# Performance work log

Measured on AMD Instinct MI355X. Metric: run time of the kernel, lower is better.

## Reference

```python
import jax, jax.numpy as jnp
import numpy as np

B, S, Lb, C, CP, H = 64, 4, 64, 32, 16, 4
LN_EPS = 1e-5


def layer_norm(x, g, b):
    mu = jnp.mean(x, axis=-1, keepdims=True)
    var = jnp.mean(jnp.square(x - mu), axis=-1, keepdims=True)
    return (x - mu) * jax.lax.rsqrt(var + LN_EPS) * g + b


def mha(x, w_in, b_in, w_out, b_out, h):
    # torch nn.MultiheadAttention, batch_first, self-attention
    Bx, L, Cx = x.shape
    d = Cx // h
    qkv = x @ w_in.T + b_in                      # (Bx, L, 3C)
    q, k, v = jnp.split(qkv, 3, axis=-1)
    sp = lambda t: t.reshape(Bx, L, h, d).transpose(0, 2, 1, 3)  # (Bx,h,L,d)
    q, k, v = sp(q), sp(k), sp(v)
    scale = 1.0 / jnp.sqrt(jnp.asarray(d, x.dtype))
    attn = jax.nn.softmax(jnp.einsum('bhid,bhjd->bhij', q, k) * scale, axis=-1)
    o = jnp.einsum('bhij,bhjd->bhid', attn, v).transpose(0, 2, 1, 3).reshape(Bx, L, Cx)
    return o @ w_out.T + b_out


def setup_inputs() -> dict:
    key = jax.random.key(0)
    ks = jax.random.split(key, 20)
    g = lambda i, shape, s=0.05: (jax.random.normal(ks[i], shape, dtype=jnp.float32) * s)
    inp = {
        'chip_ctcf': jax.random.normal(ks[0], (B, Lb), dtype=jnp.float32),
        'chip_hac':  jax.random.normal(ks[1], (B, Lb), dtype=jnp.float32),
        'chip_me1':  jax.random.normal(ks[2], (B, Lb), dtype=jnp.float32),
        'chip_me3':  jax.random.normal(ks[3], (B, Lb), dtype=jnp.float32),
        'embed_w': g(4, (C, 1)), 'embed_b': g(5, (C,)),
        'pos_embed': g(6, (1, 1, Lb, C), 0.02),
        'row_in_w': g(7, (3 * C, C)), 'row_in_b': g(8, (3 * C,)),
        'row_out_w': g(9, (C, C)), 'row_out_b': g(10, (C,)),
        'row_ln_g': jnp.ones((C,), jnp.float32), 'row_ln_b': jnp.zeros((C,), jnp.float32),
        'col_in_w': g(11, (3 * C, C)), 'col_in_b': g(12, (3 * C,)),
        'col_out_w': g(13, (C, C)), 'col_out_b': g(14, (C,)),
        'col_ln_g': jnp.ones((C,), jnp.float32), 'col_ln_b': jnp.zeros((C,), jnp.float32),
        'proj_w': g(15, (CP, C * C)), 'proj_b': g(16, (CP,)),
        'pln_g': jnp.ones((CP,), jnp.float32), 'pln_b': jnp.zeros((CP,), jnp.float32),
    }
    return inp


def reference(chip_ctcf, chip_hac, chip_me1, chip_me3,
              embed_w, embed_b, pos_embed,
              row_in_w, row_in_b, row_out_w, row_out_b, row_ln_g, row_ln_b,
              col_in_w, col_in_b, col_out_w, col_out_b, col_ln_g, col_ln_b,
              proj_w, proj_b, pln_g, pln_b):
    Bv = chip_ctcf.shape[0]
    signals = jnp.stack([chip_ctcf, chip_hac, chip_me1, chip_me3], axis=1)  # (B,4,64)
    # Linear(1, C): scalar embed
    msa = signals[..., None] * embed_w[:, 0] + embed_b                      # (B,4,64,C)
    msa = msa + pos_embed
    # row attention over the 64 bins, per track
    x = msa.reshape(Bv * S, Lb, C)
    x = layer_norm(x + mha(x, row_in_w, row_in_b, row_out_w, row_out_b, H), row_ln_g, row_ln_b)
    msa = x.reshape(Bv, S, Lb, C)
    # column attention over the 4 tracks, per bin
    x = msa.transpose(0, 2, 1, 3).reshape(Bv * Lb, S, C)
    x = layer_norm(x + mha(x, col_in_w, col_in_b, col_out_w, col_out_b, H), col_ln_g, col_ln_b)
    msa = x.reshape(Bv, Lb, S, C).transpose(0, 2, 1, 3)                     # (B,4,64,C)
    # outer product of the track-mean (as written in the torch source)
    m = jnp.mean(msa, axis=1)                                               # (B,64,C)
    pair = jnp.einsum('bic,bjd->bijcd', m, m).reshape(Bv, Lb, Lb, C * C)    # (B,64,64,1024)
    nrm = jnp.sqrt(jnp.sum(jnp.square(pair), axis=-1, keepdims=True))
    pair = pair / jnp.maximum(nrm, 1e-6)                                    # F.normalize eps=1e-6
    feat = pair @ proj_w.T + proj_b                                         # (B,64,64,CP)
    feat = layer_norm(feat, pln_g, pln_b)
    feat = feat * jax.nn.sigmoid(feat)                                      # SiLU
    return feat.transpose(0, 3, 1, 2)                                       # (B,CP,64,64)
```

## Files before the change

kernel.cpp:

```cpp
#include <hip/hip_runtime.h>

#define LN_EPS 1e-5f

__device__ __forceinline__ float dot8(float4 a0, float4 a1, float4 b0, float4 b1) {
    return a0.x * b0.x + a0.y * b0.y + a0.z * b0.z + a0.w * b0.w +
           a1.x * b1.x + a1.y * b1.y + a1.z * b1.z + a1.w * b1.w;
}

__global__ __launch_bounds__(1024) void k_row(
    const float* __restrict__ ctcf, const float* __restrict__ hac,
    const float* __restrict__ me1,  const float* __restrict__ me3,
    const float* __restrict__ ew,   const float* __restrict__ eb,
    const float* __restrict__ pe,
    const float* __restrict__ w_in, const float* __restrict__ b_in,
    const float* __restrict__ w_out,const float* __restrict__ b_out,
    const float* __restrict__ ln_g, const float* __restrict__ ln_b,
    float* __restrict__ msaR)
{
    __shared__ float sx[64][33];
    __shared__ float sqkv[64 * 100];
    __shared__ float so[64][33];
    __shared__ float smean[64], srstd[64];

    const int blk = blockIdx.x;
    const int s   = blk & 3;
    const int b   = blk >> 2;
    const int tid = threadIdx.x;

    const float* chip = (s == 0) ? ctcf : (s == 1) ? hac : (s == 2) ? me1 : me3;

    for (int n = tid; n < 2048; n += 1024) {
        int l = n >> 5, c = n & 31;
        sx[l][c] = chip[b * 64 + l] * ew[c] + eb[c] + pe[l * 32 + c];
    }
    __syncthreads();

    const int l  = tid & 63;
    const int cg = tid >> 6;

    {
        float xr[32];
#pragma unroll
        for (int c = 0; c < 32; ++c) xr[c] = sx[l][c];
#pragma unroll
        for (int i = 0; i < 6; ++i) {
            int cc = i * 16 + cg;
            const float4* wr4 = (const float4*)&w_in[cc * 32];
            float acc = b_in[cc];
#pragma unroll
            for (int c4 = 0; c4 < 8; ++c4) {
                float4 wv = wr4[c4];
                acc += xr[c4 * 4 + 0] * wv.x + xr[c4 * 4 + 1] * wv.y +
                       xr[c4 * 4 + 2] * wv.z + xr[c4 * 4 + 3] * wv.w;
            }
            sqkv[l * 100 + cc] = acc;
        }
    }
    __syncthreads();

    {
        const int h  = tid >> 8;
        const int la = (tid >> 2) & 63;
        const int kc = tid & 3;
        const float4* qp = (const float4*)&sqkv[la * 100 + h * 8];
        float4 q0 = qp[0], q1 = qp[1];
        const float scale = 0.35355339059327373f;
        float mrun = -1e30f, denom = 0.f, a[8];
#pragma unroll
        for (int dd = 0; dd < 8; ++dd) a[dd] = 0.f;
#pragma unroll
        for (int jj = 0; jj < 16; ++jj) {
            const int j = kc * 16 + jj;
            const float4* kp = (const float4*)&sqkv[j * 100 + 32 + h * 8];
            float sc = dot8(q0, q1, kp[0], kp[1]) * scale;
            const float4* vp = (const float4*)&sqkv[j * 100 + 64 + h * 8];
            float4 v0 = vp[0], v1 = vp[1];
            float mnew = fmaxf(mrun, sc);
            float corr = __expf(mrun - mnew);
            float w = __expf(sc - mnew);
            denom = denom * corr + w;
            a[0] = a[0] * corr + w * v0.x;  a[1] = a[1] * corr + w * v0.y;
            a[2] = a[2] * corr + w * v0.z;  a[3] = a[3] * corr + w * v0.w;
            a[4] = a[4] * corr + w * v1.x;  a[5] = a[5] * corr + w * v1.y;
            a[6] = a[6] * corr + w * v1.z;  a[7] = a[7] * corr + w * v1.w;
            mrun = mnew;
        }
#pragma unroll
        for (int off = 1; off <= 2; off <<= 1) {
            float mo = __shfl_xor(mrun, off, 64);
            float dn = __shfl_xor(denom, off, 64);
            float mn = fmaxf(mrun, mo);
            float c1 = __expf(mrun - mn);
            float c2 = __expf(mo - mn);
            denom = denom * c1 + dn * c2;
#pragma unroll
            for (int dd = 0; dd < 8; ++dd) {
                float ao = __shfl_xor(a[dd], off, 64);
                a[dd] = a[dd] * c1 + ao * c2;
            }
            mrun = mn;
        }
        float inv = 1.f / denom;
        float r0, r1;
        if      (kc == 0) { r0 = a[0]; r1 = a[1]; }
        else if (kc == 1) { r0 = a[2]; r1 = a[3]; }
        else if (kc == 2) { r0 = a[4]; r1 = a[5]; }
        else              { r0 = a[6]; r1 = a[7]; }
        so[la][h * 8 + kc * 2 + 0] = r0 * inv;
        so[la][h * 8 + kc * 2 + 1] = r1 * inv;
    }
    __syncthreads();

    {
        float orow[32];
#pragma unroll
        for (int k = 0; k < 32; ++k) orow[k] = so[l][k];
#pragma unroll
        for (int i = 0; i < 2; ++i) {
            int c = i * 16 + cg;
            const float4* wr4 = (const float4*)&w_out[c * 32];
            float acc = b_out[c] + sx[l][c];
#pragma unroll
            for (int k4 = 0; k4 < 8; ++k4) {
                float4 wv = wr4[k4];
                acc += orow[k4 * 4 + 0] * wv.x + orow[k4 * 4 + 1] * wv.y +
                       orow[k4 * 4 + 2] * wv.z + orow[k4 * 4 + 3] * wv.w;
            }
            sqkv[l * 100 + c] = acc;
        }
    }
    __syncthreads();

    if (tid < 64) {
        float mu = 0.f;
#pragma unroll
        for (int c = 0; c < 32; ++c) mu += sqkv[tid * 100 + c];
        mu *= (1.f / 32.f);
        float var = 0.f;
#pragma unroll
        for (int c = 0; c < 32; ++c) { float d = sqkv[tid * 100 + c] - mu; var += d * d; }
        var *= (1.f / 32.f);
        smean[tid] = mu;
        srstd[tid] = rsqrtf(var + LN_EPS);
    }
    __syncthreads();

    float* outp = msaR + blk * 2048;
    for (int n = tid; n < 2048; n += 1024) {
        int ll = n >> 5, c = n & 31;
        outp[n] = (sqkv[ll * 100 + c] - smean[ll]) * srstd[ll] * ln_g[c] + ln_b[c];
    }
}

__global__ __launch_bounds__(1024) void k_col(
    const float* __restrict__ msaR,
    const float* __restrict__ w_in, const float* __restrict__ b_in,
    const float* __restrict__ w_out,const float* __restrict__ b_out,
    const float* __restrict__ ln_g, const float* __restrict__ ln_b,
    float* __restrict__ m_out, float* __restrict__ nrm_out)
{
    __shared__ float sx[64][33];
    __shared__ float sqkv[64 * 100];
    __shared__ float so[64][33];
    __shared__ float smean2[64], srstd2[64];
    __shared__ float smv[16][33];

    const int bx = blockIdx.x;
    const int b  = bx >> 2;
    const int l0 = (bx & 3) * 16;
    const int tid = threadIdx.x;

    for (int n = tid; n < 2048; n += 1024) {
        int s = n >> 9, lo = (n >> 5) & 15, c = n & 31;
        sx[s * 16 + lo][c] = msaR[((b * 4 + s) * 64 + l0 + lo) * 32 + c];
    }
    __syncthreads();

    const int r  = tid & 63;
    const int sS = r & 3, lo = r >> 2;
    const int cg = tid >> 6;

    {
        float xr[32];
#pragma unroll
        for (int c = 0; c < 32; ++c) xr[c] = sx[sS * 16 + lo][c];
#pragma unroll
        for (int i = 0; i < 6; ++i) {
            int cc = i * 16 + cg;
            const float4* wr4 = (const float4*)&w_in[cc * 32];
            float acc = b_in[cc];
#pragma unroll
            for (int c4 = 0; c4 < 8; ++c4) {
                float4 wv = wr4[c4];
                acc += xr[c4 * 4 + 0] * wv.x + xr[c4 * 4 + 1] * wv.y +
                       xr[c4 * 4 + 2] * wv.z + xr[c4 * 4 + 3] * wv.w;
            }
            sqkv[r * 100 + cc] = acc;
        }
    }
    __syncthreads();

    if (tid < 256) {
        const int la = tid >> 4, h = (tid >> 2) & 3, ia = tid & 3;
        const float scale = 0.35355339059327373f;
        const float4* qp = (const float4*)&sqkv[(la * 4 + ia) * 100 + h * 8];
        float4 q0 = qp[0], q1 = qp[1];
        float sc[4];
        float mx = -1e30f;
#pragma unroll
        for (int jj = 0; jj < 4; ++jj) {
            const float4* kp = (const float4*)&sqkv[(la * 4 + jj) * 100 + 32 + h * 8];
            sc[jj] = dot8(q0, q1, kp[0], kp[1]) * scale;
            mx = fmaxf(mx, sc[jj]);
        }
        float den = 0.f;
#pragma unroll
        for (int jj = 0; jj < 4; ++jj) { sc[jj] = __expf(sc[jj] - mx); den += sc[jj]; }
        float inv = 1.f / den;
        float a[8];
#pragma unroll
        for (int dd = 0; dd < 8; ++dd) a[dd] = 0.f;
#pragma unroll
        for (int jj = 0; jj < 4; ++jj) {
            const float4* vp = (const float4*)&sqkv[(la * 4 + jj) * 100 + 64 + h * 8];
            float4 v0 = vp[0], v1 = vp[1];
            float wgt = sc[jj];
            a[0] += wgt * v0.x;  a[1] += wgt * v0.y;
            a[2] += wgt * v0.z;  a[3] += wgt * v0.w;
            a[4] += wgt * v1.x;  a[5] += wgt * v1.y;
            a[6] += wgt * v1.z;  a[7] += wgt * v1.w;
        }
#pragma unroll
        for (int dd = 0; dd < 8; ++dd) so[la * 4 + ia][h * 8 + dd] = a[dd] * inv;
    }
    __syncthreads();

    {
        float orow[32];
#pragma unroll
        for (int k = 0; k < 32; ++k) orow[k] = so[r][k];
#pragma unroll
        for (int i = 0; i < 2; ++i) {
            int c = i * 16 + cg;
            const float4* wr4 = (const float4*)&w_out[c * 32];
            float acc = b_out[c] + sx[sS * 16 + lo][c];
#pragma unroll
            for (int k4 = 0; k4 < 8; ++k4) {
                float4 wv = wr4[k4];
                acc += orow[k4 * 4 + 0] * wv.x + orow[k4 * 4 + 1] * wv.y +
                       orow[k4 * 4 + 2] * wv.z + orow[k4 * 4 + 3] * wv.w;
            }
            sqkv[r * 100 + c] = acc;
        }
    }
    __syncthreads();

    if (tid < 64) {
        float mu = 0.f;
#pragma unroll
        for (int c = 0; c < 32; ++c) mu += sqkv[tid * 100 + c];
        mu *= (1.f / 32.f);
        float var = 0.f;
#pragma unroll
        for (int c = 0; c < 32; ++c) { float d = sqkv[tid * 100 + c] - mu; var += d * d; }
        var *= (1.f / 32.f);
        smean2[tid] = mu;
        srstd2[tid] = rsqrtf(var + LN_EPS);
    }
    __syncthreads();

    if (tid < 512) {
        int loo = tid >> 5, c = tid & 31;
        float acc = 0.f;
#pragma unroll
        for (int ss = 0; ss < 4; ++ss) {
            int rr = loo * 4 + ss;
            acc += (sqkv[rr * 100 + c] - smean2[rr]) * srstd2[rr];
        }
        float mval = 0.25f * acc * ln_g[c] + ln_b[c];
        m_out[(b * 64 + l0 + loo) * 32 + c] = mval;
        smv[loo][c] = mval * mval;
    }
    __syncthreads();

    if (tid < 16) {
        float sum = 0.f;
#pragma unroll
        for (int c = 0; c < 32; ++c) sum += smv[tid][c];
        nrm_out[b * 64 + l0 + tid] = sqrtf(sum);
    }
}

__global__ __launch_bounds__(512, 4) void k_pair(
    const float* __restrict__ m, const float* __restrict__ nrm,
    const float* __restrict__ pw, const float* __restrict__ pb,
    const float* __restrict__ pg, const float* __restrict__ pbeta,
    float* __restrict__ out)
{
    __shared__ float smj[64][36];
    __shared__ float sT[8 * 520];
    __shared__ float snj[64];
    __shared__ float sbias[16], sgam[16], sbet[16];

    const int bx = blockIdx.x;
    const int b  = bx >> 3;
    const int i0 = (bx & 7) * 8;
    const int tid = threadIdx.x;
    const int lane = tid & 63, w = tid >> 6;

    const int rem = tid;
    const float* pwp = pw + (rem >> 5) * 1024 + (rem & 31);
    float w0[32];
#pragma unroll
    for (int c = 0; c < 32; ++c) w0[c] = pwp[c * 32];

    const float* mb = m + b * 2048;
    for (int n = tid; n < 2048; n += 512) smj[n >> 5][n & 31] = mb[n];
    if (tid < 64) snj[tid] = nrm[b * 64 + tid];
    if (tid < 16) {
        sbias[tid] = pb[tid];
        sgam[tid]  = pg[tid];
        sbet[tid]  = pbeta[tid];
    }
    __syncthreads();

#pragma unroll
    for (int il = 0; il < 8; ++il) {
        const float4* mr4 = (const float4*)&smj[i0 + il][0];
        float a0 = 0.f;
#pragma unroll
        for (int c4 = 0; c4 < 8; ++c4) {
            float4 mv = mr4[c4];
            a0 += mv.x * w0[c4 * 4 + 0] + mv.y * w0[c4 * 4 + 1] +
                  mv.z * w0[c4 * 4 + 2] + mv.w * w0[c4 * 4 + 3];
        }
        sT[il * 520 + rem] = a0;
    }
    __syncthreads();

    const int j = lane;
    float mj[32];
    {
        const float4* mjp = (const float4*)&smj[j][0];
#pragma unroll
        for (int d4 = 0; d4 < 8; ++d4) {
            float4 t = mjp[d4];
            mj[d4 * 4 + 0] = t.x;  mj[d4 * 4 + 1] = t.y;
            mj[d4 * 4 + 2] = t.z;  mj[d4 * 4 + 3] = t.w;
        }
    }
    const float nj = snj[j];

    {
        const int il = w;
        const int ig = i0 + il;
        const float invn = 1.f / fmaxf(snj[ig] * nj, 1e-6f);
        float f[16];
#pragma unroll
        for (int cp = 0; cp < 16; ++cp) {
            const float4* tr = (const float4*)&sT[il * 520 + cp * 32];
            float acc = 0.f;
#pragma unroll
            for (int d4 = 0; d4 < 8; ++d4) {
                float4 tv = tr[d4];
                acc += tv.x * mj[d4 * 4 + 0] + tv.y * mj[d4 * 4 + 1] +
                       tv.z * mj[d4 * 4 + 2] + tv.w * mj[d4 * 4 + 3];
            }
            f[cp] = acc * invn + sbias[cp];
        }
        float mu = 0.f;
#pragma unroll
        for (int cp = 0; cp < 16; ++cp) mu += f[cp];
        mu *= (1.f / 16.f);
        float var = 0.f;
#pragma unroll
        for (int cp = 0; cp < 16; ++cp) { float d = f[cp] - mu; var += d * d; }
        var *= (1.f / 16.f);
        const float rstd = rsqrtf(var + LN_EPS);
#pragma unroll
        for (int cp = 0; cp < 16; ++cp) {
            float v = (f[cp] - mu) * rstd * sgam[cp] + sbet[cp];
            float sl = v / (1.f + __expf(-v));
            out[((b * 16 + cp) * 64 + ig) * 64 + j] = sl;
        }
    }
}

extern "C" void kernel_launch(void* const* d_in, const int* in_sizes, int n_in,
                              void* d_out, int out_size, void* d_ws, size_t ws_size,
                              hipStream_t stream) {
    const float* ctcf  = (const float*)d_in[0];
    const float* hac   = (const float*)d_in[1];
    const float* me1   = (const float*)d_in[2];
    const float* me3   = (const float*)d_in[3];
    const float* ew    = (const float*)d_in[4];
    const float* ebias = (const float*)d_in[5];
    const float* pe    = (const float*)d_in[6];
    const float* riw   = (const float*)d_in[7];
    const float* rib   = (const float*)d_in[8];
    const float* row_  = (const float*)d_in[9];
    const float* rob   = (const float*)d_in[10];
    const float* rlg   = (const float*)d_in[11];
    const float* rlb   = (const float*)d_in[12];
    const float* ciw   = (const float*)d_in[13];
    const float* cib   = (const float*)d_in[14];
    const float* cow   = (const float*)d_in[15];
    const float* cob   = (const float*)d_in[16];
    const float* clg   = (const float*)d_in[17];
    const float* clb   = (const float*)d_in[18];
    const float* pw    = (const float*)d_in[19];
    const float* pb    = (const float*)d_in[20];
    const float* pg    = (const float*)d_in[21];
    const float* pbt   = (const float*)d_in[22];

    float* out = (float*)d_out;

    float* msaR = (float*)d_out;
    float* mbuf = (float*)d_ws;
    float* nbuf = mbuf + 64 * 64 * 32;

    k_row<<<256, 1024, 0, stream>>>(ctcf, hac, me1, me3, ew, ebias, pe,
                                    riw, rib, row_, rob, rlg, rlb, msaR);
    k_col<<<256, 1024, 0, stream>>>(msaR, ciw, cib, cow, cob, clg, clb,
                                    mbuf, nbuf);
    k_pair<<<512, 512, 0, stream>>>(mbuf, nbuf, pw, pb, pg, pbt, out);
}
```

Measured before the change: 149.2 us.

## Split all three kernels into smaller blocks and use shuffle-based layer norm

```diff
diff --git a/kernel.cpp b/kernel.cpp
--- a/kernel.cpp
+++ b/kernel.cpp
@@ -7,7 +7,7 @@
            a1.x * b1.x + a1.y * b1.y + a1.z * b1.z + a1.w * b1.w;
 }
 
-__global__ __launch_bounds__(1024) void k_row(
+__global__ __launch_bounds__(512, 4) void k_row(
     const float* __restrict__ ctcf, const float* __restrict__ hac,
     const float* __restrict__ me1,  const float* __restrict__ me3,
     const float* __restrict__ ew,   const float* __restrict__ eb,
@@ -19,32 +19,32 @@
 {
     __shared__ float sx[64][33];
     __shared__ float sqkv[64 * 100];
-    __shared__ float so[64][33];
-    __shared__ float smean[64], srstd[64];
+    __shared__ float so[32][33];
 
     const int blk = blockIdx.x;
-    const int s   = blk & 3;
-    const int b   = blk >> 2;
+    const int qh  = blk & 1;
+    const int s   = (blk >> 1) & 3;
+    const int b   = blk >> 3;
+    const int qbase = qh * 32;
     const int tid = threadIdx.x;
 
     const float* chip = (s == 0) ? ctcf : (s == 1) ? hac : (s == 2) ? me1 : me3;
 
-    for (int n = tid; n < 2048; n += 1024) {
+    for (int n = tid; n < 2048; n += 512) {
         int l = n >> 5, c = n & 31;
         sx[l][c] = chip[b * 64 + l] * ew[c] + eb[c] + pe[l * 32 + c];
     }
     __syncthreads();
 
-    const int l  = tid & 63;
-    const int cg = tid >> 6;
-
-    {
+    {
+        const int l  = tid & 63;
+        const int cg = tid >> 6;
         float xr[32];
 #pragma unroll
         for (int c = 0; c < 32; ++c) xr[c] = sx[l][c];
 #pragma unroll
-        for (int i = 0; i < 6; ++i) {
-            int cc = i * 16 + cg;
+        for (int i = 0; i < 12; ++i) {
+            int cc = i * 8 + cg;
             const float4* wr4 = (const float4*)&w_in[cc * 32];
             float acc = b_in[cc];
 #pragma unroll
@@ -59,10 +59,11 @@
     __syncthreads();
 
     {
-        const int h  = tid >> 8;
-        const int la = (tid >> 2) & 63;
+        const int h  = tid >> 7;
+        const int q  = (tid >> 2) & 31;
         const int kc = tid & 3;
-        const float4* qp = (const float4*)&sqkv[la * 100 + h * 8];
+        const int lq = qbase + q;
+        const float4* qp = (const float4*)&sqkv[lq * 100 + h * 8];
         float4 q0 = qp[0], q1 = qp[1];
         const float scale = 0.35355339059327373f;
         float mrun = -1e30f, denom = 0.f, a[8];
@@ -70,7 +71,7 @@
         for (int dd = 0; dd < 8; ++dd) a[dd] = 0.f;
 #pragma unroll
         for (int jj = 0; jj < 16; ++jj) {
-            const int j = kc * 16 + jj;
+            const int j = kc * 16 + ((jj + kc) & 15);
             const float4* kp = (const float4*)&sqkv[j * 100 + 32 + h * 8];
             float sc = dot8(q0, q1, kp[0], kp[1]) * scale;
             const float4* vp = (const float4*)&sqkv[j * 100 + 64 + h * 8];
@@ -106,84 +107,82 @@
         else if (kc == 1) { r0 = a[2]; r1 = a[3]; }
         else if (kc == 2) { r0 = a[4]; r1 = a[5]; }
         else              { r0 = a[6]; r1 = a[7]; }
-        so[la][h * 8 + kc * 2 + 0] = r0 * inv;
-        so[la][h * 8 + kc * 2 + 1] = r1 * inv;
-    }
-    __syncthreads();
-
-    {
+        so[q][h * 8 + kc * 2 + 0] = r0 * inv;
+        so[q][h * 8 + kc * 2 + 1] = r1 * inv;
+    }
+    __syncthreads();
+
+    {
+        const int lq2 = tid & 31;
+        const int cB  = tid >> 5;
         float orow[32];
 #pragma unroll
-        for (int k = 0; k < 32; ++k) orow[k] = so[l][k];
+        for (int k = 0; k < 32; ++k) orow[k] = so[lq2][k];
 #pragma unroll
         for (int i = 0; i < 2; ++i) {
-            int c = i * 16 + cg;
+            int c = cB + i * 16;
             const float4* wr4 = (const float4*)&w_out[c * 32];
-            float acc = b_out[c] + sx[l][c];
+            float acc = b_out[c] + sx[qbase + lq2][c];
 #pragma unroll
             for (int k4 = 0; k4 < 8; ++k4) {
                 float4 wv = wr4[k4];
                 acc += orow[k4 * 4 + 0] * wv.x + orow[k4 * 4 + 1] * wv.y +
                        orow[k4 * 4 + 2] * wv.z + orow[k4 * 4 + 3] * wv.w;
             }
-            sqkv[l * 100 + c] = acc;
-        }
-    }
-    __syncthreads();
-
-    if (tid < 64) {
-        float mu = 0.f;
-#pragma unroll
-        for (int c = 0; c < 32; ++c) mu += sqkv[tid * 100 + c];
-        mu *= (1.f / 32.f);
-        float var = 0.f;
-#pragma unroll
-        for (int c = 0; c < 32; ++c) { float d = sqkv[tid * 100 + c] - mu; var += d * d; }
-        var *= (1.f / 32.f);
-        smean[tid] = mu;
-        srstd[tid] = rsqrtf(var + LN_EPS);
-    }
-    __syncthreads();
-
-    float* outp = msaR + blk * 2048;
-    for (int n = tid; n < 2048; n += 1024) {
-        int ll = n >> 5, c = n & 31;
-        outp[n] = (sqkv[ll * 100 + c] - smean[ll]) * srstd[ll] * ln_g[c] + ln_b[c];
+            sqkv[lq2 * 100 + c] = acc;
+        }
+    }
+    __syncthreads();
+
+    {
+        const int c = tid & 31;
+#pragma unroll
+        for (int p = 0; p < 2; ++p) {
+            int r = p * 16 + (tid >> 5);
+            float v = sqkv[r * 100 + c];
+            float s1 = v;
+#pragma unroll
+            for (int off = 16; off >= 1; off >>= 1) s1 += __shfl_xor(s1, off, 64);
+            float mu = s1 * (1.f / 32.f);
+            float d = v - mu;
+            float s2 = d * d;
+#pragma unroll
+            for (int off = 16; off >= 1; off >>= 1) s2 += __shfl_xor(s2, off, 64);
+            float rstd = rsqrtf(s2 * (1.f / 32.f) + LN_EPS);
+            msaR[((b * 4 + s) * 64 + qbase + r) * 32 + c] = d * rstd * ln_g[c] + ln_b[c];
+        }
     }
 }
 
-__global__ __launch_bounds__(1024) void k_col(
+__global__ __launch_bounds__(512, 4) void k_col(
     const float* __restrict__ msaR,
     const float* __restrict__ w_in, const float* __restrict__ b_in,
     const float* __restrict__ w_out,const float* __restrict__ b_out,
     const float* __restrict__ ln_g, const float* __restrict__ ln_b,
     float* __restrict__ m_out, float* __restrict__ nrm_out)
 {
-    __shared__ float sx[64][33];
-    __shared__ float sqkv[64 * 100];
-    __shared__ float so[64][33];
-    __shared__ float smean2[64], srstd2[64];
-    __shared__ float smv[16][33];
+    __shared__ float sx[32][33];
+    __shared__ float sqkv[32 * 100];
+    __shared__ float so[32][33];
 
     const int bx = blockIdx.x;
-    const int b  = bx >> 2;
-    const int l0 = (bx & 3) * 16;
+    const int b  = bx >> 3;
+    const int l0 = (bx & 7) * 8;
     const int tid = threadIdx.x;
 
-    for (int n = tid; n < 2048; n += 1024) {
-        int s = n >> 9, lo = (n >> 5) & 15, c = n & 31;
-        sx[s * 16 + lo][c] = msaR[((b * 4 + s) * 64 + l0 + lo) * 32 + c];
-    }
-    __syncthreads();
-
-    const int r  = tid & 63;
-    const int sS = r & 3, lo = r >> 2;
-    const int cg = tid >> 6;
-
-    {
+    for (int n = tid; n < 1024; n += 512) {
+        int r = n >> 5, c = n & 31;
+        int lo = r >> 2, s = r & 3;
+        sx[r][c] = msaR[((b * 4 + s) * 64 + l0 + lo) * 32 + c];
+    }
+    __syncthreads();
+
+    {
+        const int rr = tid & 31;
+        const int cg = tid >> 5;
         float xr[32];
 #pragma unroll
-        for (int c = 0; c < 32; ++c) xr[c] = sx[sS * 16 + lo][c];
+        for (int c = 0; c < 32; ++c) xr[c] = sx[rr][c];
 #pragma unroll
         for (int i = 0; i < 6; ++i) {
             int cc = i * 16 + cg;
@@ -195,21 +194,21 @@
                 acc += xr[c4 * 4 + 0] * wv.x + xr[c4 * 4 + 1] * wv.y +
                        xr[c4 * 4 + 2] * wv.z + xr[c4 * 4 + 3] * wv.w;
             }
-            sqkv[r * 100 + cc] = acc;
-        }
-    }
-    __syncthreads();
-
-    if (tid < 256) {
-        const int la = tid >> 4, h = (tid >> 2) & 3, ia = tid & 3;
+            sqkv[rr * 100 + cc] = acc;
+        }
+    }
+    __syncthreads();
+
+    if (tid < 128) {
+        const int lo = tid >> 4, h = (tid >> 2) & 3, ia = tid & 3;
         const float scale = 0.35355339059327373f;
-        const float4* qp = (const float4*)&sqkv[(la * 4 + ia) * 100 + h * 8];
+        const float4* qp = (const float4*)&sqkv[(lo * 4 + ia) * 100 + h * 8];
         float4 q0 = qp[0], q1 = qp[1];
         float sc[4];
         float mx = -1e30f;
 #pragma unroll
         for (int jj = 0; jj < 4; ++jj) {
-            const float4* kp = (const float4*)&sqkv[(la * 4 + jj) * 100 + 32 + h * 8];
+            const float4* kp = (const float4*)&sqkv[(lo * 4 + jj) * 100 + 32 + h * 8];
             sc[jj] = dot8(q0, q1, kp[0], kp[1]) * scale;
             mx = fmaxf(mx, sc[jj]);
         }
@@ -222,7 +221,7 @@
         for (int dd = 0; dd < 8; ++dd) a[dd] = 0.f;
 #pragma unroll
         for (int jj = 0; jj < 4; ++jj) {
-            const float4* vp = (const float4*)&sqkv[(la * 4 + jj) * 100 + 64 + h * 8];
+            const float4* vp = (const float4*)&sqkv[(lo * 4 + jj) * 100 + 64 + h * 8];
             float4 v0 = vp[0], v1 = vp[1];
             float wgt = sc[jj];
             a[0] += wgt * v0.x;  a[1] += wgt * v0.y;
@@ -231,91 +230,90 @@
             a[6] += wgt * v1.z;  a[7] += wgt * v1.w;
         }
 #pragma unroll
-        for (int dd = 0; dd < 8; ++dd) so[la * 4 + ia][h * 8 + dd] = a[dd] * inv;
-    }
-    __syncthreads();
-
-    {
+        for (int dd = 0; dd < 8; ++dd) so[lo * 4 + ia][h * 8 + dd] = a[dd] * inv;
+    }
+    __syncthreads();
+
+    {
+        const int r2 = tid & 31;
+        const int cB = tid >> 5;
         float orow[32];
 #pragma unroll
-        for (int k = 0; k < 32; ++k) orow[k] = so[r][k];
+        for (int k = 0; k < 32; ++k) orow[k] = so[r2][k];
 #pragma unroll
         for (int i = 0; i < 2; ++i) {
-            int c = i * 16 + cg;
+            int c = cB + i * 16;
             const float4* wr4 = (const float4*)&w_out[c * 32];
-            float acc = b_out[c] + sx[sS * 16 + lo][c];
+            float acc = b_out[c] + sx[r2][c];
 #pragma unroll
             for (int k4 = 0; k4 < 8; ++k4) {
                 float4 wv = wr4[k4];
                 acc += orow[k4 * 4 + 0] * wv.x + orow[k4 * 4 + 1] * wv.y +
                        orow[k4 * 4 + 2] * wv.z + orow[k4 * 4 + 3] * wv.w;
             }
-            sqkv[r * 100 + c] = acc;
-        }
-    }
-    __syncthreads();
-
-    if (tid < 64) {
-        float mu = 0.f;
-#pragma unroll
-        for (int c = 0; c < 32; ++c) mu += sqkv[tid * 100 + c];
-        mu *= (1.f / 32.f);
-        float var = 0.f;
-#pragma unroll
-        for (int c = 0; c < 32; ++c) { float d = sqkv[tid * 100 + c] - mu; var += d * d; }
-        var *= (1.f / 32.f);
-        smean2[tid] = mu;
-        srstd2[tid] = rsqrtf(var + LN_EPS);
-    }
-    __syncthreads();
-
-    if (tid < 512) {
-        int loo = tid >> 5, c = tid & 31;
-        float acc = 0.f;
-#pragma unroll
-        for (int ss = 0; ss < 4; ++ss) {
-            int rr = loo * 4 + ss;
-            acc += (sqkv[rr * 100 + c] - smean2[rr]) * srstd2[rr];
-        }
-        float mval = 0.25f * acc * ln_g[c] + ln_b[c];
-        m_out[(b * 64 + l0 + loo) * 32 + c] = mval;
-        smv[loo][c] = mval * mval;
-    }
-    __syncthreads();
-
-    if (tid < 16) {
-        float sum = 0.f;
-#pragma unroll
-        for (int c = 0; c < 32; ++c) sum += smv[tid][c];
-        nrm_out[b * 64 + l0 + tid] = sqrtf(sum);
+            sqkv[r2 * 100 + c] = acc;
+        }
+    }
+    __syncthreads();
+
+    {
+        const int c = tid & 31;
+#pragma unroll
+        for (int p = 0; p < 2; ++p) {
+            int r = p * 16 + (tid >> 5);
+            float v = sqkv[r * 100 + c];
+            float s1 = v;
+#pragma unroll
+            for (int off = 16; off >= 1; off >>= 1) s1 += __shfl_xor(s1, off, 64);
+            float mu = s1 * (1.f / 32.f);
+            float d = v - mu;
+            float s2 = d * d;
+#pragma unroll
+            for (int off = 16; off >= 1; off >>= 1) s2 += __shfl_xor(s2, off, 64);
+            float rstd = rsqrtf(s2 * (1.f / 32.f) + LN_EPS);
+            so[r][c] = d * rstd;
+        }
+    }
+    __syncthreads();
+
+    if (tid < 256) {
+        const int lo = tid >> 5, c = tid & 31;
+        float mval = 0.25f * (so[lo * 4 + 0][c] + so[lo * 4 + 1][c] +
+                              so[lo * 4 + 2][c] + so[lo * 4 + 3][c]) * ln_g[c] + ln_b[c];
+        m_out[(b * 64 + l0 + lo) * 32 + c] = mval;
+        float q2 = mval * mval;
+#pragma unroll
+        for (int off = 16; off >= 1; off >>= 1) q2 += __shfl_xor(q2, off, 64);
+        if (c == 0) nrm_out[b * 64 + l0 + lo] = sqrtf(q2);
     }
 }
 
-__global__ __launch_bounds__(512, 4) void k_pair(
+__global__ __launch_bounds__(256, 4) void k_pair(
     const float* __restrict__ m, const float* __restrict__ nrm,
     const float* __restrict__ pw, const float* __restrict__ pb,
     const float* __restrict__ pg, const float* __restrict__ pbeta,
     float* __restrict__ out)
 {
     __shared__ float smj[64][36];
-    __shared__ float sT[8 * 520];
+    __shared__ float sT[4 * 520];
     __shared__ float snj[64];
     __shared__ float sbias[16], sgam[16], sbet[16];
 
     const int bx = blockIdx.x;
-    const int b  = bx >> 3;
-    const int i0 = (bx & 7) * 8;
+    const int b  = bx >> 4;
+    const int i0 = (bx & 15) * 4;
     const int tid = threadIdx.x;
     const int lane = tid & 63, w = tid >> 6;
 
-    const int rem = tid;
-    const float* pwp = pw + (rem >> 5) * 1024 + (rem & 31);
-    float w0[32];
-#pragma unroll
-    for (int c = 0; c < 32; ++c) w0[c] = pwp[c * 32];
+    const int rem0 = tid, rem1 = tid + 256;
+    const float* pw0 = pw + (rem0 >> 5) * 1024 + (rem0 & 31);
+    const float* pw1 = pw + (rem1 >> 5) * 1024 + (rem1 & 31);
+    float w0[32], w1[32];
+#pragma unroll
+    for (int c = 0; c < 32; ++c) { w0[c] = pw0[c * 32]; w1[c] = pw1[c * 32]; }
 
     const float* mb = m + b * 2048;
-    for (int n = tid; n < 2048; n += 512) smj[n >> 5][n & 31] = mb[n];
+    for (int n = tid; n < 2048; n += 256) smj[n >> 5][n & 31] = mb[n];
     if (tid < 64) snj[tid] = nrm[b * 64 + tid];
     if (tid < 16) {
         sbias[tid] = pb[tid];
@@ -325,16 +323,19 @@
     __syncthreads();
 
 #pragma unroll
-    for (int il = 0; il < 8; ++il) {
+    for (int il = 0; il < 4; ++il) {
         const float4* mr4 = (const float4*)&smj[i0 + il][0];
-        float a0 = 0.f;
+        float a0 = 0.f, a1 = 0.f;
 #pragma unroll
         for (int c4 = 0; c4 < 8; ++c4) {
             float4 mv = mr4[c4];
             a0 += mv.x * w0[c4 * 4 + 0] + mv.y * w0[c4 * 4 + 1] +
                   mv.z * w0[c4 * 4 + 2] + mv.w * w0[c4 * 4 + 3];
-        }
-        sT[il * 520 + rem] = a0;
+            a1 += mv.x * w1[c4 * 4 + 0] + mv.y * w1[c4 * 4 + 1] +
+                  mv.z * w1[c4 * 4 + 2] + mv.w * w1[c4 * 4 + 3];
+        }
+        sT[il * 520 + rem0] = a0;
+        sT[il * 520 + rem1] = a1;
     }
     __syncthreads();
 
@@ -419,9 +420,9 @@
     float* mbuf = (float*)d_ws;
     float* nbuf = mbuf + 64 * 64 * 32;
 
-    k_row<<<256, 1024, 0, stream>>>(ctcf, hac, me1, me3, ew, ebias, pe,
-                                    riw, rib, row_, rob, rlg, rlb, msaR);
-    k_col<<<256, 1024, 0, stream>>>(msaR, ciw, cib, cow, cob, clg, clb,
-                                    mbuf, nbuf);
-    k_pair<<<512, 512, 0, stream>>>(mbuf, nbuf, pw, pb, pg, pbt, out);
+    k_row<<<512, 512, 0, stream>>>(ctcf, hac, me1, me3, ew, ebias, pe,
+                                   riw, rib, row_, rob, rlg, rlb, msaR);
+    k_col<<<512, 512, 0, stream>>>(msaR, ciw, cib, cow, cob, clg, clb,
+                                   mbuf, nbuf);
+    k_pair<<<1024, 256, 0, stream>>>(mbuf, nbuf, pw, pb, pg, pbt, out);
 }
```

After: 144.4 us. 3.3% less time.
